# Performance work log

Hardware: AMD Instinct MI355X
Metric: run time of the kernel (lower is better)

Reference implementation:

```python
import jax, jax.numpy as jnp
import numpy as np

F, H, NSEQ, T, A, LP, LV = 256, 256, 64, 2048, 32, 512, 512
N = NSEQ * T


def setup_inputs() -> dict:
    key = jax.random.key(0)
    ks = jax.random.split(key, 24)
    p = lambda k, shape: jax.random.normal(k, shape, jnp.float32) * 0.05
    return {
        'features': jax.random.normal(ks[0], (N, F), jnp.float32),
        'episode_starts': (jax.random.uniform(ks[1], (N,)) < 0.005).astype(jnp.float32),
        'h_pi': jax.random.normal(ks[2], (1, NSEQ, H), jnp.float32),
        'c_pi': jax.random.normal(ks[3], (1, NSEQ, H), jnp.float32),
        'h_vf': jax.random.normal(ks[4], (1, NSEQ, H), jnp.float32),
        'c_vf': jax.random.normal(ks[5], (1, NSEQ, H), jnp.float32),
        'W_feat': p(ks[6], (4 * F, F)), 'b_feat': jnp.zeros((4 * F,), jnp.float32),
        'W_emb': p(ks[7], (H, F)), 'b_emb': jnp.zeros((H,), jnp.float32),
        'W_ih': p(ks[8], (4 * H, F)), 'W_hh': p(ks[9], (4 * H, H)),
        'b_ih': jnp.zeros((4 * H,), jnp.float32), 'b_hh': jnp.zeros((4 * H,), jnp.float32),
        'Wp1': p(ks[10], (LP, H + 3 * F)), 'bp1': jnp.zeros((LP,), jnp.float32),
        'Wp2': p(ks[11], (A, LP)), 'bp2': jnp.zeros((A,), jnp.float32),
        'Wv1': p(ks[12], (LV, H + 3 * F)), 'bv1': jnp.zeros((LV,), jnp.float32),
        'Wv2': p(ks[13], (1, LV)), 'bv2': jnp.zeros((1,), jnp.float32),
    }


def _lstm_masked_scan(feats, starts, h0, c0, W_ih, W_hh, b_ih, b_hh):
    # feats: (T, n_seq, F), starts: (T, n_seq); PyTorch gate order i,f,g,o
    xg = jnp.einsum('tnf,gf->tng', feats, W_ih) + b_ih  # precompute input gates

    def step(carry, xs):
        h, c = carry
        xg_t, s_t = xs
        m = (1.0 - s_t)[:, None]          # episode-reset mask
        h = h * m
        c = c * m
        g = xg_t + h @ W_hh.T + b_hh
        i, f, gg, o = jnp.split(g, 4, axis=-1)
        c = jax.nn.sigmoid(f) * c + jax.nn.sigmoid(i) * jnp.tanh(gg)
        h = jax.nn.sigmoid(o) * jnp.tanh(c)
        return (h, c), h

    (hT, cT), hs = jax.lax.scan(step, (h0, c0), (xg, starts))
    return hs, hT, cT


def reference(features, episode_starts, h_pi, c_pi, h_vf, c_vf,
              W_feat, b_feat, W_emb, b_emb, W_ih, W_hh, b_ih, b_hh,
              Wp1, bp1, Wp2, bp2, Wv1, bv1, Wv2, bv2):
    n_seq = h_vf.shape[1]
    feats = features.reshape(n_seq, -1, F).swapaxes(0, 1)      # (T, n_seq, F)
    starts = episode_starts.reshape(n_seq, -1).swapaxes(0, 1)  # (T, n_seq)

    feat4 = jnp.einsum('tnf,gf->tng', feats, W_feat) + b_feat  # (T, n_seq, 4F)
    f1 = feat4[..., : 3 * F]
    f1_flat = f1.swapaxes(0, 1).reshape(-1, 3 * F)             # (N, 3F)

    # actor branch: TempLSTM ignores its LSTM -> just Linear(F, H) on raw feats;
    # the loop branch feeds raw features_sequence (source behavior).
    out_pi = jnp.einsum('tnf,hf->tnh', feats, W_emb) + b_emb   # (T, n_seq, H)
    out_pi_flat = out_pi.swapaxes(0, 1).reshape(-1, H)

    # critic branch: masked LSTM recurrence with per-step episode resets
    hs, hT, cT = _lstm_masked_scan(feats, starts, h_vf[0], c_vf[0], W_ih, W_hh, b_ih, b_hh)
    hs_flat = hs.swapaxes(0, 1).reshape(-1, H)

    latent_pi = jnp.concatenate([f1_flat, out_pi_flat], axis=-1)
    latent_vf = jnp.concatenate([f1_flat, hs_flat], axis=-1)

    values = jax.nn.relu(latent_vf @ Wv1.T + bv1) @ Wv2.T + bv2      # (N, 1)
    logits = jax.nn.relu(latent_pi @ Wp1.T + bp1) @ Wp2.T + bp2      # (N, A)

    actions = jnp.argmax(logits, axis=-1)  # deterministic=True -> mode
    log_prob = jnp.take_along_axis(jax.nn.log_softmax(logits, axis=-1), actions[:, None], axis=1)[:, 0]

    # actor final state = h0 scaled by product of reset masks (loop semantics)
    mprod = jnp.prod(1.0 - starts, axis=0)[None, :, None]
    h_pi_f, c_pi_f = h_pi * mprod, c_pi * mprod
    return actions, values, log_prob, h_pi_f, c_pi_f, hT[None], cT[None]
```

## Files before the change

### kernel.cpp

```cpp
#include <hip/hip_runtime.h>
#include <stdint.h>
#include <math.h>

#define N_TOT 131072
#define TSEQ  2048
#define NSEQ  64
#define CS    128
#define NCH   16
#define PARTS 4

typedef unsigned long long u64;

__global__ __launch_bounds__(256)
void transpose_whh(const float* __restrict__ Whh, float* __restrict__ Wg)
{
    const int k = blockIdx.x;
    const int u = threadIdx.x;
#pragma unroll
    for (int g = 0; g < 4; ++g)
        Wg[(size_t)k * 1024 + u * 4 + g] = Whh[(size_t)(g * 256 + u) * 256 + k];
}

__global__ __launch_bounds__(256)
void gemm_xg(const float* __restrict__ A, const float* __restrict__ Wih,
             const float* __restrict__ bih, const float* __restrict__ bhh,
             float* __restrict__ xg, int base)
{
    __shared__ float As[16][136];
    __shared__ float Bs[16][136];
    const int t  = threadIdx.x;
    const int n0 = blockIdx.x * 128;
    const int seq = blockIdx.y;
    const size_t grow0 = (size_t)seq * TSEQ + base;
    const size_t lrow0 = (size_t)seq * CS;
    const int tx = t & 15, ty = t >> 4;

    float acc[8][8];
#pragma unroll
    for (int i = 0; i < 8; ++i)
#pragma unroll
        for (int j = 0; j < 8; ++j) acc[i][j] = 0.f;

    for (int kt = 0; kt < 256; kt += 16) {
#pragma unroll
        for (int jj = 0; jj < 2; ++jj) {
            int idx = t + 256 * jj;
            int m = idx >> 2, q = idx & 3;
            float4 a = *(const float4*)(A + (grow0 + m) * 256 + kt + q * 4);
            As[q * 4 + 0][m] = a.x; As[q * 4 + 1][m] = a.y;
            As[q * 4 + 2][m] = a.z; As[q * 4 + 3][m] = a.w;
            float4 b = *(const float4*)(Wih + (size_t)(n0 + m) * 256 + kt + q * 4);
            Bs[q * 4 + 0][m] = b.x; Bs[q * 4 + 1][m] = b.y;
            Bs[q * 4 + 2][m] = b.z; Bs[q * 4 + 3][m] = b.w;
        }
        __syncthreads();
#pragma unroll
        for (int k = 0; k < 16; ++k) {
            float4 a0 = *(const float4*)&As[k][ty * 8];
            float4 a1 = *(const float4*)&As[k][ty * 8 + 4];
            float4 b0 = *(const float4*)&Bs[k][tx * 8];
            float4 b1 = *(const float4*)&Bs[k][tx * 8 + 4];
            float av[8] = {a0.x, a0.y, a0.z, a0.w, a1.x, a1.y, a1.z, a1.w};
            float bv[8] = {b0.x, b0.y, b0.z, b0.w, b1.x, b1.y, b1.z, b1.w};
#pragma unroll
            for (int i = 0; i < 8; ++i)
#pragma unroll
                for (int j = 0; j < 8; ++j) acc[i][j] += av[i] * bv[j];
        }
        __syncthreads();
    }
#pragma unroll
    for (int i = 0; i < 8; ++i) {
        size_t lr = lrow0 + ty * 8 + i;
#pragma unroll
        for (int j = 0; j < 8; ++j) {
            int n = n0 + tx * 8 + j;
            int gate = n >> 8, u = n & 255;
            xg[lr * 1024 + u * 4 + gate] = acc[i][j] + bih[n] + bhh[n];
        }
    }
}

__device__ __forceinline__ void l2_store_u64(u64* p, u64 v)
{
    asm volatile("global_store_dwordx2 %0, %1, off"
                 :: "v"(p), "v"(v) : "memory");
}

__device__ __forceinline__ u64 l2_load_u64(const u64* p)
{
    u64 v;
    asm volatile("global_load_dwordx2 %0, %1, off sc0\n\t"
                 "s_waitcnt vmcnt(0)"
                 : "=v"(v) : "v"(p) : "memory");
    return v;
}

__global__ __launch_bounds__(1024)
void lstm4_h1p(const float* __restrict__ xg, const float* __restrict__ starts,
               const float* __restrict__ h0g, const float* __restrict__ c0g,
               float* __restrict__ hstate, float* __restrict__ cstate,
               const float* __restrict__ Wg,
               float* __restrict__ hs, float* __restrict__ hT,
               float* __restrict__ cT,
               u64* __restrict__ hx, u64* __restrict__ hx2,
               unsigned* __restrict__ fastState,
               const float* __restrict__ lat, const float* __restrict__ Wp1,
               const float* __restrict__ bp1, float* __restrict__ h1,
               int base, int fastflag)
{
    __shared__ float smem[9216];

    const int t   = threadIdx.x;
    const int bid = blockIdx.x;

    if (bid < 256) {
        float* hmask = smem;
        float* part  = smem + 256;

        const int slot = bid >> 3;
        const int seq  = (bid & 7) + 8 * (slot >> 2);
        const int p    = slot & 3;
        const int u    = t & 63;
        const int q    = t >> 6;

        float4 Wr[16];
#pragma unroll
        for (int kk = 0; kk < 16; ++kk)
            Wr[kk] = *(const float4*)(Wg + (size_t)(q * 16 + kk) * 1024 + (p * 64 + u) * 4);

        float c_reg = 0.f;
        if (t < 64) {
            const float* csrc = (base == 0) ? c0g : cstate;
            c_reg = csrc[(size_t)seq * 256 + p * 64 + t];
        }

        bool useFast = (fastflag != 0);
        if (useFast) {
            unsigned st = __hip_atomic_load(fastState, __ATOMIC_RELAXED,
                                            __HIP_MEMORY_SCOPE_AGENT);
            if (st != 0u) useFast = false;
        }

        for (int lt = 0; lt < CS; ++lt) {
            const int S = base + lt;
            const float m = 1.f - starts[(size_t)seq * TSEQ + S];

            float4 x4 = make_float4(0.f, 0.f, 0.f, 0.f);
            if (t < 64)
                x4 = *(const float4*)(xg + ((size_t)seq * CS + lt) * 1024 + (p * 64 + t) * 4);

            if (lt == 0) {
                if (t < 256) {
                    const float* hsrc = (base == 0) ? h0g : hstate;
                    hmask[t] = hsrc[(size_t)seq * 256 + t] * m;
                }
            } else {
                if (t < 256) {
                    const size_t idx = (size_t)(S & 1) * (NSEQ * 256) + (size_t)seq * 256 + t;
                    u64 w = 0;
                    if (useFast) {
                        int tries = 0;
                        for (;;) {
                            w = l2_load_u64(&hx2[idx]);
                            if ((unsigned)(w >> 32) == (unsigned)S) break;
                            if (++tries > 768) {
                                useFast = false;
                                __hip_atomic_store(fastState, 1u, __ATOMIC_RELAXED,
                                                   __HIP_MEMORY_SCOPE_AGENT);
                                break;
                            }
                        }
                    }
                    if (!useFast) {
                        unsigned spins = 0;
                        for (;;) {
                            w = __hip_atomic_load(&hx[idx], __ATOMIC_RELAXED,
                                                  __HIP_MEMORY_SCOPE_AGENT);
                            if ((unsigned)(w >> 32) == (unsigned)S) break;
                            __builtin_amdgcn_s_sleep(1);
                            if (++spins > (1u << 18)) break;
                        }
                    }
                    hmask[t] = __uint_as_float((unsigned)w) * m;
                }
            }
            __syncthreads();

            const float* hp = &hmask[q * 16];
            float4 h0 = *(const float4*)(hp + 0);
            float4 h1v_ = *(const float4*)(hp + 4);
            float4 h2 = *(const float4*)(hp + 8);
            float4 h3 = *(const float4*)(hp + 12);
            float hv[16] = {h0.x,h0.y,h0.z,h0.w, h1v_.x,h1v_.y,h1v_.z,h1v_.w,
                            h2.x,h2.y,h2.z,h2.w, h3.x,h3.y,h3.z,h3.w};
            float a0 = 0.f, a1 = 0.f, a2 = 0.f, a3 = 0.f;
#pragma unroll
            for (int kk = 0; kk < 16; ++kk) {
                a0 += hv[kk] * Wr[kk].x;
                a1 += hv[kk] * Wr[kk].y;
                a2 += hv[kk] * Wr[kk].z;
                a3 += hv[kk] * Wr[kk].w;
            }
            *(float4*)&part[(q * 64 + u) * 4] = make_float4(a0, a1, a2, a3);
            __syncthreads();

            if (t < 64) {
                float gi = 0.f, gf = 0.f, gg = 0.f, go = 0.f;
#pragma unroll
                for (int qq = 0; qq < 16; ++qq) {
                    float4 pp = *(const float4*)&part[(qq * 64 + t) * 4];
                    gi += pp.x; gf += pp.y; gg += pp.z; go += pp.w;
                }
                gi += x4.x; gf += x4.y; gg += x4.z; go += x4.w;
                float c = c_reg * m;
                float si = 1.f / (1.f + expf(-gi));
                float sf = 1.f / (1.f + expf(-gf));
                float so = 1.f / (1.f + expf(-go));
                c = sf * c + si * tanhf(gg);
                float h = so * tanhf(c);
                c_reg = c;

                const int gu = p * 64 + t;
                const size_t widx = (size_t)((S + 1) & 1) * (NSEQ * 256)
                                  + (size_t)seq * 256 + gu;
                const u64 pkt = ((u64)(unsigned)(S + 1) << 32)
                              | (u64)__float_as_uint(h);
                if (fastflag) l2_store_u64(&hx2[widx], pkt);
                __hip_atomic_store(&hx[widx], pkt,
                                   __ATOMIC_RELAXED, __HIP_MEMORY_SCOPE_AGENT);
                hs[((size_t)seq * CS + lt) * 256 + gu] = h;
                if (lt == CS - 1) {
                    cstate[(size_t)seq * 256 + gu] = c;
                    hstate[(size_t)seq * 256 + gu] = h;
                }
                if (S == TSEQ - 1) {
                    cT[(size_t)seq * 256 + gu] = c;
                    hT[(size_t)seq * 256 + gu] = h;
                }
            }
        }
    } else {
        const int s    = t >> 8;
        const int t2   = t & 255;
        const int tile = (bid - 256) * 4 + s;
        const int n0   = (tile & 7) * 64;
        const size_t lr0 = (size_t)(tile >> 3) * 64;
        float* As = smem + s * 2304;
        float* Bs = As + 1152;
        const int tx = t2 & 15, ty = t2 >> 4;

        double acc[4][4];
#pragma unroll
        for (int i = 0; i < 4; ++i)
#pragma unroll
            for (int j = 0; j < 4; ++j) acc[i][j] = 0.0;

        for (int kt = 0; kt < 1024; kt += 16) {
            {
                int m = t2 >> 2, q = t2 & 3;
                float4 a = *(const float4*)(lat + (lr0 + m) * 1024 + kt + q * 4);
                As[(q * 4 + 0) * 72 + m] = a.x; As[(q * 4 + 1) * 72 + m] = a.y;
                As[(q * 4 + 2) * 72 + m] = a.z; As[(q * 4 + 3) * 72 + m] = a.w;
                float4 b = *(const float4*)(Wp1 + (size_t)(n0 + m) * 1024 + kt + q * 4);
                Bs[(q * 4 + 0) * 72 + m] = b.x; Bs[(q * 4 + 1) * 72 + m] = b.y;
                Bs[(q * 4 + 2) * 72 + m] = b.z; Bs[(q * 4 + 3) * 72 + m] = b.w;
            }
            __syncthreads();
            float p[4][4];
#pragma unroll
            for (int i = 0; i < 4; ++i)
#pragma unroll
                for (int j = 0; j < 4; ++j) p[i][j] = 0.f;
#pragma unroll
            for (int k = 0; k < 16; ++k) {
                float4 a0 = *(const float4*)&As[k * 72 + ty * 4];
                float4 b0 = *(const float4*)&Bs[k * 72 + tx * 4];
                float av[4] = {a0.x, a0.y, a0.z, a0.w};
                float bv[4] = {b0.x, b0.y, b0.z, b0.w};
#pragma unroll
                for (int i = 0; i < 4; ++i)
#pragma unroll
                    for (int j = 0; j < 4; ++j) p[i][j] += av[i] * bv[j];
            }
#pragma unroll
            for (int i = 0; i < 4; ++i)
#pragma unroll
                for (int j = 0; j < 4; ++j) acc[i][j] += (double)p[i][j];
            __syncthreads();
        }
#pragma unroll
        for (int i = 0; i < 4; ++i) {
            size_t lr = lr0 + ty * 4 + i;
#pragma unroll
            for (int j = 0; j < 4; ++j) {
                int n = n0 + tx * 4 + j;
                float v = (float)acc[i][j] + bp1[n];
                h1[lr * 512 + n] = v > 0.f ? v : 0.f;
            }
        }
    }
}

__global__ __launch_bounds__(256)
void gemm_latent(const float* __restrict__ A, const float* __restrict__ Wfeat,
                 const float* __restrict__ Wemb, const float* __restrict__ bfeat,
                 const float* __restrict__ bemb, float* __restrict__ lat, int base)
{
    __shared__ float As[16][136];
    __shared__ float Bs[16][136];
    const int t  = threadIdx.x;
    const int n0 = blockIdx.x * 128;
    const size_t lr0 = (size_t)blockIdx.y * 128;
    const size_t grow0 = (lr0 >> 7) * TSEQ + base;
    const int tx = t & 15, ty = t >> 4;

    double acc[8][8];
#pragma unroll
    for (int i = 0; i < 8; ++i)
#pragma unroll
        for (int j = 0; j < 8; ++j) acc[i][j] = 0.0;

    for (int kt = 0; kt < 256; kt += 16) {
#pragma unroll
        for (int jj = 0; jj < 2; ++jj) {
            int idx = t + 256 * jj;
            int m = idx >> 2, q = idx & 3;
            float4 a = *(const float4*)(A + (grow0 + m) * 256 + kt + q * 4);
            As[q * 4 + 0][m] = a.x; As[q * 4 + 1][m] = a.y;
            As[q * 4 + 2][m] = a.z; As[q * 4 + 3][m] = a.w;
            int n = n0 + m;
            const float* Brow = (n < 768) ? (Wfeat + (size_t)n * 256)
                                          : (Wemb + (size_t)(n - 768) * 256);
            float4 b = *(const float4*)(Brow + kt + q * 4);
            Bs[q * 4 + 0][m] = b.x; Bs[q * 4 + 1][m] = b.y;
            Bs[q * 4 + 2][m] = b.z; Bs[q * 4 + 3][m] = b.w;
        }
        __syncthreads();
        float p[8][8];
#pragma unroll
        for (int i = 0; i < 8; ++i)
#pragma unroll
            for (int j = 0; j < 8; ++j) p[i][j] = 0.f;
#pragma unroll
        for (int k = 0; k < 16; ++k) {
            float4 a0 = *(const float4*)&As[k][ty * 8];
            float4 a1 = *(const float4*)&As[k][ty * 8 + 4];
            float4 b0 = *(const float4*)&Bs[k][tx * 8];
            float4 b1 = *(const float4*)&Bs[k][tx * 8 + 4];
            float av[8] = {a0.x, a0.y, a0.z, a0.w, a1.x, a1.y, a1.z, a1.w};
            float bv[8] = {b0.x, b0.y, b0.z, b0.w, b1.x, b1.y, b1.z, b1.w};
#pragma unroll
            for (int i = 0; i < 8; ++i)
#pragma unroll
                for (int j = 0; j < 8; ++j) p[i][j] += av[i] * bv[j];
        }
#pragma unroll
        for (int i = 0; i < 8; ++i)
#pragma unroll
            for (int j = 0; j < 8; ++j) acc[i][j] += (double)p[i][j];
        __syncthreads();
    }
#pragma unroll
    for (int i = 0; i < 8; ++i) {
        size_t lr = lr0 + ty * 8 + i;
#pragma unroll
        for (int j = 0; j < 8; ++j) {
            int n = n0 + tx * 8 + j;
            float v = (float)acc[i][j];
            v += (n < 768) ? bfeat[n] : bemb[n - 768];
            lat[lr * 1024 + n] = v;
        }
    }
}

__global__ __launch_bounds__(256)
void gemm_h1v(const float* __restrict__ lat, const float* __restrict__ hs,
              const float* __restrict__ Wv1, const float* __restrict__ bv1,
              float* __restrict__ h1)
{
    __shared__ float As[16][136];
    __shared__ float Bs[16][136];
    const int t  = threadIdx.x;
    const int n0 = blockIdx.x * 128;
    const size_t lrow0 = (size_t)blockIdx.y * 128;
    const int tx = t & 15, ty = t >> 4;

    float acc[8][8];
#pragma unroll
    for (int i = 0; i < 8; ++i)
#pragma unroll
        for (int j = 0; j < 8; ++j) acc[i][j] = 0.f;

    for (int pass = 0; pass < 2; ++pass) {
        const float* A  = (pass == 0) ? lat : hs;
        const int lda   = (pass == 0) ? 1024 : 256;
        const int kmax  = (pass == 0) ? 768 : 256;
        const int boff  = (pass == 0) ? 0 : 768;
        for (int kt = 0; kt < kmax; kt += 16) {
#pragma unroll
            for (int jj = 0; jj < 2; ++jj) {
                int idx = t + 256 * jj;
                int m = idx >> 2, q = idx & 3;
                float4 a = *(const float4*)(A + (lrow0 + m) * lda + kt + q * 4);
                As[q * 4 + 0][m] = a.x; As[q * 4 + 1][m] = a.y;
                As[q * 4 + 2][m] = a.z; As[q * 4 + 3][m] = a.w;
                float4 b = *(const float4*)(Wv1 + (size_t)(n0 + m) * 1024 + boff + kt + q * 4);
                Bs[q * 4 + 0][m] = b.x; Bs[q * 4 + 1][m] = b.y;
                Bs[q * 4 + 2][m] = b.z; Bs[q * 4 + 3][m] = b.w;
            }
            __syncthreads();
#pragma unroll
            for (int k = 0; k < 16; ++k) {
                float4 a0 = *(const float4*)&As[k][ty * 8];
                float4 a1 = *(const float4*)&As[k][ty * 8 + 4];
                float4 b0 = *(const float4*)&Bs[k][tx * 8];
                float4 b1 = *(const float4*)&Bs[k][tx * 8 + 4];
                float av[8] = {a0.x, a0.y, a0.z, a0.w, a1.x, a1.y, a1.z, a1.w};
                float bv[8] = {b0.x, b0.y, b0.z, b0.w, b1.x, b1.y, b1.z, b1.w};
#pragma unroll
                for (int i = 0; i < 8; ++i)
#pragma unroll
                    for (int j = 0; j < 8; ++j) acc[i][j] += av[i] * bv[j];
            }
            __syncthreads();
        }
    }
#pragma unroll
    for (int i = 0; i < 8; ++i) {
        size_t lr = lrow0 + ty * 8 + i;
#pragma unroll
        for (int j = 0; j < 8; ++j) {
            int n = n0 + tx * 8 + j;
            float v = acc[i][j] + bv1[n];
            h1[lr * 512 + n] = v > 0.f ? v : 0.f;
        }
    }
}

__global__ __launch_bounds__(256)
void mask_kernel(const float* __restrict__ starts, const float* __restrict__ h_pi,
                 const float* __restrict__ c_pi,
                 float* __restrict__ o_hpi, float* __restrict__ o_cpi)
{
    __shared__ float red[256];
    const int n = blockIdx.x, t = threadIdx.x;
    float a = 0.f;
    for (int j = 0; j < 8; ++j)
        a = fmaxf(a, starts[(size_t)n * TSEQ + t * 8 + j]);
    red[t] = a; __syncthreads();
    for (int s = 128; s > 0; s >>= 1) {
        if (t < s) red[t] = fmaxf(red[t], red[t + s]);
        __syncthreads();
    }
    float m = (red[0] > 0.f) ? 0.f : 1.f;
    o_hpi[(size_t)n * 256 + t] = h_pi[(size_t)n * 256 + t] * m;
    o_cpi[(size_t)n * 256 + t] = c_pi[(size_t)n * 256 + t] * m;
}

__global__ __launch_bounds__(256)
void policy_finish(const float* __restrict__ h1p, const float* __restrict__ Wp2,
                   const float* __restrict__ bp2,
                   float* __restrict__ o_actions, float* __restrict__ o_logp,
                   int base)
{
    __shared__ float w2t[512 * 32];
    const int t = threadIdx.x;
    for (int j = 0; j < 64; ++j) {
        int idx = t + 256 * j;
        int k = idx >> 5, c = idx & 31;
        w2t[idx] = Wp2[(size_t)c * 512 + k];
    }
    __syncthreads();

    const int c = t & 31;
    size_t lr = (size_t)blockIdx.x * 8 + (t >> 5);
    size_t grow = (lr >> 7) * TSEQ + base + (lr & 127);
    const float* hrow = h1p + lr * 512;
    double s = 0.0;
    for (int k = 0; k < 512; k += 4) {
        float4 h4 = *(const float4*)(hrow + k);
        s += (double)h4.x * (double)w2t[(k + 0) * 32 + c];
        s += (double)h4.y * (double)w2t[(k + 1) * 32 + c];
        s += (double)h4.z * (double)w2t[(k + 2) * 32 + c];
        s += (double)h4.w * (double)w2t[(k + 3) * 32 + c];
    }
    double logit = s + (double)bp2[c];

    double mv = logit; int mi = c;
#pragma unroll
    for (int off = 16; off >= 1; off >>= 1) {
        double ov = __shfl_xor(mv, off, 32);
        int    oi = __shfl_xor(mi, off, 32);
        if (ov > mv || (ov == mv && oi < mi)) { mv = ov; mi = oi; }
    }
    double se = exp(logit - mv);
#pragma unroll
    for (int off = 16; off >= 1; off >>= 1) se += __shfl_xor(se, off, 32);

    if (c == 0) {
        o_actions[grow] = (float)mi;
        o_logp[grow]    = (float)(-log(se));
    }
}

__global__ __launch_bounds__(256)
void value_finish(const float* __restrict__ h1v, const float* __restrict__ Wv2,
                  const float* __restrict__ bv2, float* __restrict__ o_values,
                  int base)
{
    __shared__ float wv[512];
    const int t = threadIdx.x;
    wv[t] = Wv2[t]; wv[t + 256] = Wv2[t + 256];
    __syncthreads();
    const int q = t & 3;
    size_t lr = (size_t)blockIdx.x * 64 + (t >> 2);
    size_t grow = (lr >> 7) * TSEQ + base + (lr & 127);
    const float* hrow = h1v + lr * 512;
    float s = 0.f;
    for (int k = q * 128; k < q * 128 + 128; k += 4) {
        float4 h4 = *(const float4*)(hrow + k);
        float4 w4 = *(const float4*)&wv[k];
        s += h4.x * w4.x + h4.y * w4.y + h4.z * w4.z + h4.w * w4.w;
    }
    s += __shfl_xor(s, 1, 4);
    s += __shfl_xor(s, 2, 4);
    if (q == 0) o_values[grow] = s + bv2[0];
}

extern "C" void kernel_launch(void* const* d_in, const int* in_sizes, int n_in,
                              void* d_out, int out_size, void* d_ws, size_t ws_size,
                              hipStream_t stream)
{
    const float* features = (const float*)d_in[0];
    const float* starts   = (const float*)d_in[1];
    const float* h_pi     = (const float*)d_in[2];
    const float* c_pi     = (const float*)d_in[3];
    const float* h_vf     = (const float*)d_in[4];
    const float* c_vf     = (const float*)d_in[5];
    const float* W_feat   = (const float*)d_in[6];
    const float* b_feat   = (const float*)d_in[7];
    const float* W_emb    = (const float*)d_in[8];
    const float* b_emb    = (const float*)d_in[9];
    const float* W_ih     = (const float*)d_in[10];
    const float* W_hh     = (const float*)d_in[11];
    const float* b_ih     = (const float*)d_in[12];
    const float* b_hh     = (const float*)d_in[13];
    const float* Wp1      = (const float*)d_in[14];
    const float* bp1      = (const float*)d_in[15];
    const float* Wp2      = (const float*)d_in[16];
    const float* bp2      = (const float*)d_in[17];
    const float* Wv1      = (const float*)d_in[18];
    const float* bv1      = (const float*)d_in[19];
    const float* Wv2      = (const float*)d_in[20];
    const float* bv2      = (const float*)d_in[21];

    float* out = (float*)d_out;
    float* o_actions = out;
    float* o_values  = out + N_TOT;
    float* o_logp    = out + 2 * (size_t)N_TOT;
    float* o_hpi     = out + 3 * (size_t)N_TOT;
    float* o_cpi     = o_hpi + NSEQ * 256;
    float* o_hT      = o_cpi + NSEQ * 256;
    float* o_cT      = o_hT  + NSEQ * 256;

    char* ws = (char*)d_ws;
    const size_t MB = 1024 * 1024;
    float* xg_c  = (float*)(ws);
    float* lat_c = (float*)(ws + 32 * MB);
    float* hs_c  = (float*)(ws + 64 * MB);
    float* h1_c  = (float*)(ws + 72 * MB);
    float* Wg    = (float*)(ws + 88 * MB);
    float* hstate = (float*)(ws + 89 * MB);
    float* cstate = (float*)(ws + 89 * MB + 65536);
    u64*   hx     = (u64*)  (ws + 89 * MB + 131072);
    u64*   hx2    = (u64*)  (ws + 89 * MB + 393216);
    unsigned* fastState = (unsigned*)(ws + 89 * MB + 655360);

    const int fastflag = (ws_size >= 89 * MB + 656 * 1024) ? 1 : 0;
    u64* hx2_eff = fastflag ? hx2 : hx;
    unsigned* fs_eff = fastflag ? fastState : (unsigned*)hx;

    transpose_whh<<<256, 256, 0, stream>>>(W_hh, Wg);

    mask_kernel<<<NSEQ, 256, 0, stream>>>(starts, h_pi, c_pi, o_hpi, o_cpi);

    for (int c = 0; c < NCH; ++c) {
        const int base = c * CS;

        gemm_xg<<<dim3(8, NSEQ), 256, 0, stream>>>(features, W_ih, b_ih, b_hh,
                                                   xg_c, base);
        gemm_latent<<<dim3(8, 64), 256, 0, stream>>>(
            features, W_feat, W_emb, b_feat, b_emb, lat_c, base);

        lstm4_h1p<<<512, 1024, 0, stream>>>(xg_c, starts, h_vf, c_vf,
                                            hstate, cstate, Wg,
                                            hs_c, o_hT, o_cT, hx, hx2_eff,
                                            fs_eff,
                                            lat_c, Wp1, bp1, h1_c,
                                            base, fastflag);

        policy_finish<<<1024, 256, 0, stream>>>(h1_c, Wp2, bp2,
                                                o_actions, o_logp, base);

        gemm_h1v<<<dim3(4, 64), 256, 0, stream>>>(lat_c, hs_c, Wv1, bv1, h1_c);
        value_finish<<<128, 256, 0, stream>>>(h1_c, Wv2, bv2, o_values, base);
    }
}
```

Measured before the change: 14.74 ms.

## Fold value-head feature weights, fuse xg/latent GEMMs, raise recurrence priority

Precomputes Wv1[:, :768] @ W_feat and the matching bias once, so the value-head first layer uses a K=256 pass over raw features plus a K=256 pass over hs instead of K=1024 over the latent. Merges the xg and latent GEMMs into one launch by splitting on block index. Raises wave priority for the LSTM recurrence blocks and gives each policy_finish block four rows to process. The fold changes the float rounding order in the value path, and it only runs when the workspace is at least 91 MB.

Result: no change. 14.86 ms (+0.8%).

```diff
diff --git a/kernel.cpp b/kernel.cpp
--- a/kernel.cpp
+++ b/kernel.cpp
@@ -22,62 +22,21 @@
 }
 
 __global__ __launch_bounds__(256)
-void gemm_xg(const float* __restrict__ A, const float* __restrict__ Wih,
-             const float* __restrict__ bih, const float* __restrict__ bhh,
-             float* __restrict__ xg, int base)
-{
-    __shared__ float As[16][136];
-    __shared__ float Bs[16][136];
-    const int t  = threadIdx.x;
-    const int n0 = blockIdx.x * 128;
-    const int seq = blockIdx.y;
-    const size_t grow0 = (size_t)seq * TSEQ + base;
-    const size_t lrow0 = (size_t)seq * CS;
-    const int tx = t & 15, ty = t >> 4;
-
-    float acc[8][8];
-#pragma unroll
-    for (int i = 0; i < 8; ++i)
-#pragma unroll
-        for (int j = 0; j < 8; ++j) acc[i][j] = 0.f;
-
-    for (int kt = 0; kt < 256; kt += 16) {
-#pragma unroll
-        for (int jj = 0; jj < 2; ++jj) {
-            int idx = t + 256 * jj;
-            int m = idx >> 2, q = idx & 3;
-            float4 a = *(const float4*)(A + (grow0 + m) * 256 + kt + q * 4);
-            As[q * 4 + 0][m] = a.x; As[q * 4 + 1][m] = a.y;
-            As[q * 4 + 2][m] = a.z; As[q * 4 + 3][m] = a.w;
-            float4 b = *(const float4*)(Wih + (size_t)(n0 + m) * 256 + kt + q * 4);
-            Bs[q * 4 + 0][m] = b.x; Bs[q * 4 + 1][m] = b.y;
-            Bs[q * 4 + 2][m] = b.z; Bs[q * 4 + 3][m] = b.w;
-        }
-        __syncthreads();
-#pragma unroll
-        for (int k = 0; k < 16; ++k) {
-            float4 a0 = *(const float4*)&As[k][ty * 8];
-            float4 a1 = *(const float4*)&As[k][ty * 8 + 4];
-            float4 b0 = *(const float4*)&Bs[k][tx * 8];
-            float4 b1 = *(const float4*)&Bs[k][tx * 8 + 4];
-            float av[8] = {a0.x, a0.y, a0.z, a0.w, a1.x, a1.y, a1.z, a1.w};
-            float bv[8] = {b0.x, b0.y, b0.z, b0.w, b1.x, b1.y, b1.z, b1.w};
-#pragma unroll
-            for (int i = 0; i < 8; ++i)
-#pragma unroll
-                for (int j = 0; j < 8; ++j) acc[i][j] += av[i] * bv[j];
-        }
-        __syncthreads();
-    }
-#pragma unroll
-    for (int i = 0; i < 8; ++i) {
-        size_t lr = lrow0 + ty * 8 + i;
-#pragma unroll
-        for (int j = 0; j < 8; ++j) {
-            int n = n0 + tx * 8 + j;
-            int gate = n >> 8, u = n & 255;
-            xg[lr * 1024 + u * 4 + gate] = acc[i][j] + bih[n] + bhh[n];
-        }
+void prep_value(const float* __restrict__ Wv1, const float* __restrict__ Wfeat,
+                const float* __restrict__ bfeat, const float* __restrict__ bv1,
+                float* __restrict__ Wcv, float* __restrict__ bcv)
+{
+    const int n = blockIdx.x;
+    const int j = threadIdx.x;
+    double s = 0.0;
+    for (int k = 0; k < 768; ++k)
+        s += (double)Wv1[(size_t)n * 1024 + k] * (double)Wfeat[(size_t)k * 256 + j];
+    Wcv[(size_t)n * 256 + j] = (float)s;
+    if (j == 0) {
+        double b = (double)bv1[n];
+        for (int k = 0; k < 768; ++k)
+            b += (double)Wv1[(size_t)n * 1024 + k] * (double)bfeat[k];
+        bcv[n] = (float)b;
     }
 }
 
@@ -94,6 +53,130 @@
                  "s_waitcnt vmcnt(0)"
                  : "=v"(v) : "v"(p) : "memory");
     return v;
+}
+
+__global__ __launch_bounds__(256)
+void gemm_xglat(const float* __restrict__ A,
+                const float* __restrict__ Wih, const float* __restrict__ bih,
+                const float* __restrict__ bhh, float* __restrict__ xg,
+                const float* __restrict__ Wfeat, const float* __restrict__ Wemb,
+                const float* __restrict__ bfeat, const float* __restrict__ bemb,
+                float* __restrict__ lat, int base)
+{
+    __shared__ float As[16][136];
+    __shared__ float Bs[16][136];
+    const int t  = threadIdx.x;
+    const int seq = blockIdx.y;
+    const size_t grow0 = (size_t)seq * TSEQ + base;
+    const size_t lrow0 = (size_t)seq * CS;
+    const int tx = t & 15, ty = t >> 4;
+
+    if (blockIdx.x < 8) {
+        const int n0 = blockIdx.x * 128;
+        float acc[8][8];
+#pragma unroll
+        for (int i = 0; i < 8; ++i)
+#pragma unroll
+            for (int j = 0; j < 8; ++j) acc[i][j] = 0.f;
+
+        for (int kt = 0; kt < 256; kt += 16) {
+#pragma unroll
+            for (int jj = 0; jj < 2; ++jj) {
+                int idx = t + 256 * jj;
+                int m = idx >> 2, q = idx & 3;
+                float4 a = *(const float4*)(A + (grow0 + m) * 256 + kt + q * 4);
+                As[q * 4 + 0][m] = a.x; As[q * 4 + 1][m] = a.y;
+                As[q * 4 + 2][m] = a.z; As[q * 4 + 3][m] = a.w;
+                float4 b = *(const float4*)(Wih + (size_t)(n0 + m) * 256 + kt + q * 4);
+                Bs[q * 4 + 0][m] = b.x; Bs[q * 4 + 1][m] = b.y;
+                Bs[q * 4 + 2][m] = b.z; Bs[q * 4 + 3][m] = b.w;
+            }
+            __syncthreads();
+#pragma unroll
+            for (int k = 0; k < 16; ++k) {
+                float4 a0 = *(const float4*)&As[k][ty * 8];
+                float4 a1 = *(const float4*)&As[k][ty * 8 + 4];
+                float4 b0 = *(const float4*)&Bs[k][tx * 8];
+                float4 b1 = *(const float4*)&Bs[k][tx * 8 + 4];
+                float av[8] = {a0.x, a0.y, a0.z, a0.w, a1.x, a1.y, a1.z, a1.w};
+                float bv[8] = {b0.x, b0.y, b0.z, b0.w, b1.x, b1.y, b1.z, b1.w};
+#pragma unroll
+                for (int i = 0; i < 8; ++i)
+#pragma unroll
+                    for (int j = 0; j < 8; ++j) acc[i][j] += av[i] * bv[j];
+            }
+            __syncthreads();
+        }
+#pragma unroll
+        for (int i = 0; i < 8; ++i) {
+            size_t lr = lrow0 + ty * 8 + i;
+#pragma unroll
+            for (int j = 0; j < 8; ++j) {
+                int n = n0 + tx * 8 + j;
+                int gate = n >> 8, u = n & 255;
+                xg[lr * 1024 + u * 4 + gate] = acc[i][j] + bih[n] + bhh[n];
+            }
+        }
+    } else {
+        const int n0 = (blockIdx.x - 8) * 128;
+        double acc[8][8];
+#pragma unroll
+        for (int i = 0; i < 8; ++i)
+#pragma unroll
+            for (int j = 0; j < 8; ++j) acc[i][j] = 0.0;
+
+        for (int kt = 0; kt < 256; kt += 16) {
+#pragma unroll
+            for (int jj = 0; jj < 2; ++jj) {
+                int idx = t + 256 * jj;
+                int m = idx >> 2, q = idx & 3;
+                float4 a = *(const float4*)(A + (grow0 + m) * 256 + kt + q * 4);
+                As[q * 4 + 0][m] = a.x; As[q * 4 + 1][m] = a.y;
+                As[q * 4 + 2][m] = a.z; As[q * 4 + 3][m] = a.w;
+                int n = n0 + m;
+                const float* Brow = (n < 768) ? (Wfeat + (size_t)n * 256)
+                                              : (Wemb + (size_t)(n - 768) * 256);
+                float4 b = *(const float4*)(Brow + kt + q * 4);
+                Bs[q * 4 + 0][m] = b.x; Bs[q * 4 + 1][m] = b.y;
+                Bs[q * 4 + 2][m] = b.z; Bs[q * 4 + 3][m] = b.w;
+            }
+            __syncthreads();
+            float p[8][8];
+#pragma unroll
+            for (int i = 0; i < 8; ++i)
+#pragma unroll
+                for (int j = 0; j < 8; ++j) p[i][j] = 0.f;
+#pragma unroll
+            for (int k = 0; k < 16; ++k) {
+                float4 a0 = *(const float4*)&As[k][ty * 8];
+                float4 a1 = *(const float4*)&As[k][ty * 8 + 4];
+                float4 b0 = *(const float4*)&Bs[k][tx * 8];
+                float4 b1 = *(const float4*)&Bs[k][tx * 8 + 4];
+                float av[8] = {a0.x, a0.y, a0.z, a0.w, a1.x, a1.y, a1.z, a1.w};
+                float bv[8] = {b0.x, b0.y, b0.z, b0.w, b1.x, b1.y, b1.z, b1.w};
+#pragma unroll
+                for (int i = 0; i < 8; ++i)
+#pragma unroll
+                    for (int j = 0; j < 8; ++j) p[i][j] += av[i] * bv[j];
+            }
+#pragma unroll
+            for (int i = 0; i < 8; ++i)
+#pragma unroll
+                for (int j = 0; j < 8; ++j) acc[i][j] += (double)p[i][j];
+            __syncthreads();
+        }
+#pragma unroll
+        for (int i = 0; i < 8; ++i) {
+            size_t lr = lrow0 + ty * 8 + i;
+#pragma unroll
+            for (int j = 0; j < 8; ++j) {
+                int n = n0 + tx * 8 + j;
+                float v = (float)acc[i][j];
+                v += (n < 768) ? bfeat[n] : bemb[n - 768];
+                lat[lr * 1024 + n] = v;
+            }
+        }
+    }
 }
 
 __global__ __launch_bounds__(1024)
@@ -115,6 +198,7 @@
     const int bid = blockIdx.x;
 
     if (bid < 256) {
+        __builtin_amdgcn_s_setprio(1);
         float* hmask = smem;
         float* part  = smem + 256;
 
@@ -189,10 +273,10 @@
 
             const float* hp = &hmask[q * 16];
             float4 h0 = *(const float4*)(hp + 0);
-            float4 h1v_ = *(const float4*)(hp + 4);
+            float4 h1f = *(const float4*)(hp + 4);
             float4 h2 = *(const float4*)(hp + 8);
             float4 h3 = *(const float4*)(hp + 12);
-            float hv[16] = {h0.x,h0.y,h0.z,h0.w, h1v_.x,h1v_.y,h1v_.z,h1v_.w,
+            float hv[16] = {h0.x,h0.y,h0.z,h0.w, h1f.x,h1f.y,h1f.z,h1f.w,
                             h2.x,h2.y,h2.z,h2.w, h3.x,h3.y,h3.z,h3.w};
             float a0 = 0.f, a1 = 0.f, a2 = 0.f, a3 = 0.f;
 #pragma unroll
@@ -303,73 +387,68 @@
 }
 
 __global__ __launch_bounds__(256)
-void gemm_latent(const float* __restrict__ A, const float* __restrict__ Wfeat,
-                 const float* __restrict__ Wemb, const float* __restrict__ bfeat,
-                 const float* __restrict__ bemb, float* __restrict__ lat, int base)
+void gemm_h1v_fold(const float* __restrict__ feats, const float* __restrict__ hs,
+                   const float* __restrict__ Wcv, const float* __restrict__ Wv1,
+                   const float* __restrict__ bcv, float* __restrict__ h1,
+                   int base)
 {
     __shared__ float As[16][136];
     __shared__ float Bs[16][136];
     const int t  = threadIdx.x;
     const int n0 = blockIdx.x * 128;
-    const size_t lr0 = (size_t)blockIdx.y * 128;
-    const size_t grow0 = (lr0 >> 7) * TSEQ + base;
+    const size_t lrow0 = (size_t)blockIdx.y * 128;
+    const size_t grow0 = (lrow0 >> 7) * TSEQ + base;
     const int tx = t & 15, ty = t >> 4;
 
-    double acc[8][8];
+    float acc[8][8];
 #pragma unroll
     for (int i = 0; i < 8; ++i)
 #pragma unroll
-        for (int j = 0; j < 8; ++j) acc[i][j] = 0.0;
-
-    for (int kt = 0; kt < 256; kt += 16) {
-#pragma unroll
-        for (int jj = 0; jj < 2; ++jj) {
-            int idx = t + 256 * jj;
-            int m = idx >> 2, q = idx & 3;
-            float4 a = *(const float4*)(A + (grow0 + m) * 256 + kt + q * 4);
-            As[q * 4 + 0][m] = a.x; As[q * 4 + 1][m] = a.y;
-            As[q * 4 + 2][m] = a.z; As[q * 4 + 3][m] = a.w;
-            int n = n0 + m;
-            const float* Brow = (n < 768) ? (Wfeat + (size_t)n * 256)
-                                          : (Wemb + (size_t)(n - 768) * 256);
-            float4 b = *(const float4*)(Brow + kt + q * 4);
-            Bs[q * 4 + 0][m] = b.x; Bs[q * 4 + 1][m] = b.y;
-            Bs[q * 4 + 2][m] = b.z; Bs[q * 4 + 3][m] = b.w;
-        }
-        __syncthreads();
-        float p[8][8];
-#pragma unroll
-        for (int i = 0; i < 8; ++i)
-#pragma unroll
-            for (int j = 0; j < 8; ++j) p[i][j] = 0.f;
-#pragma unroll
-        for (int k = 0; k < 16; ++k) {
-            float4 a0 = *(const float4*)&As[k][ty * 8];
-            float4 a1 = *(const float4*)&As[k][ty * 8 + 4];
-            float4 b0 = *(const float4*)&Bs[k][tx * 8];
-            float4 b1 = *(const float4*)&Bs[k][tx * 8 + 4];
-            float av[8] = {a0.x, a0.y, a0.z, a0.w, a1.x, a1.y, a1.z, a1.w};
-            float bv[8] = {b0.x, b0.y, b0.z, b0.w, b1.x, b1.y, b1.z, b1.w};
-#pragma unroll
-            for (int i = 0; i < 8; ++i)
-#pragma unroll
-                for (int j = 0; j < 8; ++j) p[i][j] += av[i] * bv[j];
-        }
-#pragma unroll
-        for (int i = 0; i < 8; ++i)
-#pragma unroll
-            for (int j = 0; j < 8; ++j) acc[i][j] += (double)p[i][j];
-        __syncthreads();
+        for (int j = 0; j < 8; ++j) acc[i][j] = 0.f;
+
+    for (int pass = 0; pass < 2; ++pass) {
+        const float* Abase = (pass == 0) ? (feats + grow0 * 256)
+                                         : (hs + lrow0 * 256);
+        const float* B     = (pass == 0) ? Wcv : Wv1;
+        const int ldb      = (pass == 0) ? 256 : 1024;
+        const int boff     = (pass == 0) ? 0 : 768;
+        for (int kt = 0; kt < 256; kt += 16) {
+#pragma unroll
+            for (int jj = 0; jj < 2; ++jj) {
+                int idx = t + 256 * jj;
+                int m = idx >> 2, q = idx & 3;
+                float4 a = *(const float4*)(Abase + (size_t)m * 256 + kt + q * 4);
+                As[q * 4 + 0][m] = a.x; As[q * 4 + 1][m] = a.y;
+                As[q * 4 + 2][m] = a.z; As[q * 4 + 3][m] = a.w;
+                float4 b = *(const float4*)(B + (size_t)(n0 + m) * ldb + boff + kt + q * 4);
+                Bs[q * 4 + 0][m] = b.x; Bs[q * 4 + 1][m] = b.y;
+                Bs[q * 4 + 2][m] = b.z; Bs[q * 4 + 3][m] = b.w;
+            }
+            __syncthreads();
+#pragma unroll
+            for (int k = 0; k < 16; ++k) {
+                float4 a0 = *(const float4*)&As[k][ty * 8];
+                float4 a1 = *(const float4*)&As[k][ty * 8 + 4];
+                float4 b0 = *(const float4*)&Bs[k][tx * 8];
+                float4 b1 = *(const float4*)&Bs[k][tx * 8 + 4];
+                float av[8] = {a0.x, a0.y, a0.z, a0.w, a1.x, a1.y, a1.z, a1.w};
+                float bv[8] = {b0.x, b0.y, b0.z, b0.w, b1.x, b1.y, b1.z, b1.w};
+#pragma unroll
+                for (int i = 0; i < 8; ++i)
+#pragma unroll
+                    for (int j = 0; j < 8; ++j) acc[i][j] += av[i] * bv[j];
+            }
+            __syncthreads();
+        }
     }
 #pragma unroll
     for (int i = 0; i < 8; ++i) {
-        size_t lr = lr0 + ty * 8 + i;
+        size_t lr = lrow0 + ty * 8 + i;
 #pragma unroll
         for (int j = 0; j < 8; ++j) {
             int n = n0 + tx * 8 + j;
-            float v = (float)acc[i][j];
-            v += (n < 768) ? bfeat[n] : bemb[n - 768];
-            lat[lr * 1024 + n] = v;
+            float v = acc[i][j] + bcv[n];
+            h1[lr * 512 + n] = v > 0.f ? v : 0.f;
         }
     }
 }
@@ -474,33 +553,36 @@
     __syncthreads();
 
     const int c = t & 31;
-    size_t lr = (size_t)blockIdx.x * 8 + (t >> 5);
-    size_t grow = (lr >> 7) * TSEQ + base + (lr & 127);
-    const float* hrow = h1p + lr * 512;
-    double s = 0.0;
-    for (int k = 0; k < 512; k += 4) {
-        float4 h4 = *(const float4*)(hrow + k);
-        s += (double)h4.x * (double)w2t[(k + 0) * 32 + c];
-        s += (double)h4.y * (double)w2t[(k + 1) * 32 + c];
-        s += (double)h4.z * (double)w2t[(k + 2) * 32 + c];
-        s += (double)h4.w * (double)w2t[(k + 3) * 32 + c];
-    }
-    double logit = s + (double)bp2[c];
-
-    double mv = logit; int mi = c;
-#pragma unroll
-    for (int off = 16; off >= 1; off >>= 1) {
-        double ov = __shfl_xor(mv, off, 32);
-        int    oi = __shfl_xor(mi, off, 32);
-        if (ov > mv || (ov == mv && oi < mi)) { mv = ov; mi = oi; }
-    }
-    double se = exp(logit - mv);
-#pragma unroll
-    for (int off = 16; off >= 1; off >>= 1) se += __shfl_xor(se, off, 32);
-
-    if (c == 0) {
-        o_actions[grow] = (float)mi;
-        o_logp[grow]    = (float)(-log(se));
+    const int g = t >> 5;
+    for (int it = 0; it < 4; ++it) {
+        size_t lr = (size_t)blockIdx.x * 32 + it * 8 + g;
+        size_t grow = (lr >> 7) * TSEQ + base + (lr & 127);
+        const float* hrow = h1p + lr * 512;
+        double s = 0.0;
+        for (int k = 0; k < 512; k += 4) {
+            float4 h4 = *(const float4*)(hrow + k);
+            s += (double)h4.x * (double)w2t[(k + 0) * 32 + c];
+            s += (double)h4.y * (double)w2t[(k + 1) * 32 + c];
+            s += (double)h4.z * (double)w2t[(k + 2) * 32 + c];
+            s += (double)h4.w * (double)w2t[(k + 3) * 32 + c];
+        }
+        double logit = s + (double)bp2[c];
+
+        double mv = logit; int mi = c;
+#pragma unroll
+        for (int off = 16; off >= 1; off >>= 1) {
+            double ov = __shfl_xor(mv, off, 32);
+            int    oi = __shfl_xor(mi, off, 32);
+            if (ov > mv || (ov == mv && oi < mi)) { mv = ov; mi = oi; }
+        }
+        double se = exp(logit - mv);
+#pragma unroll
+        for (int off = 16; off >= 1; off >>= 1) se += __shfl_xor(se, off, 32);
+
+        if (c == 0) {
+            o_actions[grow] = (float)mi;
+            o_logp[grow]    = (float)(-log(se));
+        }
     }
 }
 
@@ -576,22 +658,25 @@
     u64*   hx     = (u64*)  (ws + 89 * MB + 131072);
     u64*   hx2    = (u64*)  (ws + 89 * MB + 393216);
     unsigned* fastState = (unsigned*)(ws + 89 * MB + 655360);
+    float* Wcv = (float*)(ws + 89 * MB + 660480);
+    float* bcv = (float*)(ws + 89 * MB + 660480 + 524288);
 
     const int fastflag = (ws_size >= 89 * MB + 656 * 1024) ? 1 : 0;
+    const int foldflag = (ws_size >= 91 * MB) ? 1 : 0;
     u64* hx2_eff = fastflag ? hx2 : hx;
     unsigned* fs_eff = fastflag ? fastState : (unsigned*)hx;
 
     transpose_whh<<<256, 256, 0, stream>>>(W_hh, Wg);
-
+    if (foldflag)
+        prep_value<<<512, 256, 0, stream>>>(Wv1, W_feat, b_feat, bv1, Wcv, bcv);
     mask_kernel<<<NSEQ, 256, 0, stream>>>(starts, h_pi, c_pi, o_hpi, o_cpi);
 
     for (int c = 0; c < NCH; ++c) {
         const int base = c * CS;
 
-        gemm_xg<<<dim3(8, NSEQ), 256, 0, stream>>>(features, W_ih, b_ih, b_hh,
-                                                   xg_c, base);
-        gemm_latent<<<dim3(8, 64), 256, 0, stream>>>(
-            features, W_feat, W_emb, b_feat, b_emb, lat_c, base);
+        gemm_xglat<<<dim3(16, NSEQ), 256, 0, stream>>>(
+            features, W_ih, b_ih, b_hh, xg_c,
+            W_feat, W_emb, b_feat, b_emb, lat_c, base);
 
         lstm4_h1p<<<512, 1024, 0, stream>>>(xg_c, starts, h_vf, c_vf,
                                             hstate, cstate, Wg,
@@ -600,10 +685,16 @@
                                             lat_c, Wp1, bp1, h1_c,
                                             base, fastflag);
 
-        policy_finish<<<1024, 256, 0, stream>>>(h1_c, Wp2, bp2,
-                                                o_actions, o_logp, base);
-
-        gemm_h1v<<<dim3(4, 64), 256, 0, stream>>>(lat_c, hs_c, Wv1, bv1, h1_c);
+        policy_finish<<<256, 256, 0, stream>>>(h1_c, Wp2, bp2,
+                                               o_actions, o_logp, base);
+
+        if (foldflag)
+            gemm_h1v_fold<<<dim3(4, 64), 256, 0, stream>>>(
+                features, hs_c, Wcv, Wv1, bcv, h1_c, base);
+        else
+            gemm_h1v<<<dim3(4, 64), 256, 0, stream>>>(lat_c, hs_c, Wv1, bv1,
+                                                      h1_c);
+
         value_finish<<<128, 256, 0, stream>>>(h1_c, Wv2, bv2, o_values, base);
     }
 }
```
